# Optimization experiments

Hardware: AMD Instinct MI355X
Metric: run time of the kernel (lower is better)

## Reference

```python
import jax, jax.numpy as jnp
import numpy as np

N = 100000   # nodes
E = 1600000  # edges
IN = 128     # in_dim == hidden_dim
OUT = 64
MD = 16      # motif_dim
GH = 64      # gate hidden
TAU = 1.0
EPS = 1e-5


def setup_inputs() -> dict:
    key = jax.random.key(0)
    ks = jax.random.split(key, 8)
    return {
        "x": jax.random.normal(ks[0], (N, IN), jnp.float32),
        "motif_x": jax.random.normal(ks[1], (N, MD), jnp.float32),
        "edge_index": jax.random.randint(ks[2], (2, E), 0, N, jnp.int64),
        "gate_w1": jax.random.normal(ks[3], (4 * MD, GH), jnp.float32) * 0.05,
        "gate_b1": jnp.zeros((GH,), jnp.float32),
        "gate_w2": jax.random.normal(ks[4], (GH, 1), jnp.float32) * 0.05,
        "gate_b2": jnp.zeros((1,), jnp.float32),
        "conv_w": jax.random.normal(ks[5], (2, IN, IN), jnp.float32) * 0.05,
        "conv_b": jnp.zeros((2, IN), jnp.float32),
        "ln_g": jnp.ones((2, IN), jnp.float32),
        "ln_b": jnp.zeros((2, IN), jnp.float32),
        "head_w": jax.random.normal(ks[6], (IN, OUT), jnp.float32) * 0.05,
        "head_b": jnp.zeros((OUT,), jnp.float32),
    }


def reference(x, motif_x, edge_index, gate_w1, gate_b1, gate_w2, gate_b2,
              conv_w, conv_b, ln_g, ln_b, head_w, head_b):
    src, dst = edge_index[0], edge_index[1]

    # ---- EdgeGate: gather motif feats, small MLP, sigmoid gate per edge ----
    mu = motif_x[src]                      # [E, MD]
    mv = motif_x[dst]                      # [E, MD]
    feats = jnp.concatenate([mu, mv, jnp.abs(mu - mv), mu * mv], axis=1)  # [E, 4*MD]
    h = jax.nn.relu(feats @ gate_w1 + gate_b1)
    g = (h @ gate_w2 + gate_b2)[:, 0]
    gate = jnp.clip(jax.nn.sigmoid(g / TAU), 0.0, 1.0)  # [E]

    # ---- gcn_norm with self-loops (fill weight 1.0), shared across layers ----
    loops = jnp.arange(N, dtype=src.dtype)
    src_f = jnp.concatenate([src, loops])  # [E+N]
    dst_f = jnp.concatenate([dst, loops])
    w = jnp.concatenate([gate, jnp.ones((N,), gate.dtype)])
    deg = jax.ops.segment_sum(w, dst_f, num_segments=N)
    dinv = jnp.where(deg > 0, jax.lax.rsqrt(jnp.maximum(deg, EPS * 0 + 1e-30)), 0.0)
    dinv = jnp.where(deg > 0, deg ** -0.5, 0.0)
    norm = dinv[src_f] * w * dinv[dst_f]   # [E+N]

    # ---- 2 GCN layers: lin -> scatter-add -> bias -> LN -> relu -> residual ----
    for i in range(2):
        xw = x @ conv_w[i]                                   # [N, IN]
        msg = norm[:, None] * xw[src_f]                      # [E+N, IN]
        hh = jax.ops.segment_sum(msg, dst_f, num_segments=N) + conv_b[i]
        mean = jnp.mean(hh, axis=-1, keepdims=True)
        var = jnp.mean((hh - mean) ** 2, axis=-1, keepdims=True)
        hh = (hh - mean) * jax.lax.rsqrt(var + EPS) * ln_g[i] + ln_b[i]
        hh = jax.nn.relu(hh)
        x = x + hh                                           # residual (dims match)

    return x @ head_w + head_b             # [N, OUT]
```

## Files before the change

kernel.cpp:

```cpp
#include <hip/hip_runtime.h>
#include <cstdint>
#include <cstddef>

#define NN 100000
#define NE 1600000
#define IND 128
#define OUTD 64
#define MDIM 16
#define GHID 64
#define NPART 12500

typedef __attribute__((ext_vector_type(8))) short bf8_t;
typedef __attribute__((ext_vector_type(4))) float f4_t;
typedef unsigned short ushort_t;

__device__ inline unsigned f2bf_pack(float a, float b) {
    unsigned ua = __float_as_uint(a);
    unsigned ub = __float_as_uint(b);
    unsigned ra = (ua + 0x7fffu + ((ua >> 16) & 1u)) >> 16;
    unsigned rb = (ub + 0x7fffu + ((ub >> 16) & 1u)) >> 16;
    return ra | (rb << 16);
}
__device__ inline ushort_t f2bf1(float f) {
    unsigned u = __float_as_uint(f);
    return (ushort_t)((u + 0x7fffu + ((u >> 16) & 1u)) >> 16);
}
__device__ inline float2 bf2x(unsigned u) {
    return make_float2(__uint_as_float(u << 16),
                       __uint_as_float(u & 0xffff0000u));
}

__global__ __launch_bounds__(64) void k_detect(const void* ei, int* flag) {
    const unsigned long long* p = (const unsigned long long*)ei;
    int i = threadIdx.x;
    unsigned long long v = p[(size_t)i * (NE / 64)];
    bool hi0 = (v >> 32) == 0ull;
    unsigned long long b = __ballot(hi0);
    if (i == 0) *flag = (b == ~0ull) ? 1 : 0;
}

__global__ __launch_bounds__(256) void k_init(int* count) {
    int n = blockIdx.x * 256 + threadIdx.x;
    if (n < NN) count[n] = 0;
}

__global__ __launch_bounds__(256) void k_hist(const void* __restrict__ ei,
                                              const int* __restrict__ flag,
                                              int* __restrict__ count) {
    int e = blockIdx.x * 256 + threadIdx.x;
    if (e >= NE) return;
    int d = (*flag) ? (int)((const long long*)ei)[NE + e]
                    : ((const int*)ei)[NE + e];
    atomicAdd(&count[d], 1);
}

__global__ __launch_bounds__(256) void k_cvt(const float* __restrict__ x,
                                             unsigned* __restrict__ xb) {
    int i = blockIdx.x * 256 + threadIdx.x;
    if (i >= NN * 32) return;
    float4 v = ((const float4*)x)[i];
    ((uint2*)xb)[i] = make_uint2(f2bf_pack(v.x, v.y), f2bf_pack(v.z, v.w));
}

__global__ __launch_bounds__(256) void k_prep(const float* __restrict__ cw,
                                              const float* __restrict__ hw,
                                              unsigned* __restrict__ btf) {
    int i = blockIdx.x * 256 + threadIdx.x;
    if (i >= 20480) return;
    const float* W;
    int ncols, local;
    if (i < 16384) { W = cw + (i >> 13) * 16384; ncols = 128; local = i & 8191; }
    else { W = hw; ncols = 64; local = i - 16384; }
    int w = local & 3;
    int lane = (local >> 2) & 63;
    int kk = (local >> 8) & 3;
    int nt = local >> 10;
    int n = nt * 16 + (lane & 15);
    int k = kk * 32 + (lane >> 4) * 8 + 2 * w;
    btf[i] = f2bf_pack(W[k * ncols + n], W[(k + 1) * ncols + n]);
}

__global__ __launch_bounds__(256) void k_pre(const float* __restrict__ motif,
                                             const float* __restrict__ w1,
                                             unsigned* __restrict__ Pab) {
    __shared__ float sw[16][128];
    __shared__ unsigned sout[64][65];
    int tid = threadIdx.x;
#pragma unroll
    for (int i = 0; i < 8; i++) {
        int flat = tid + 256 * i;
        int k = flat >> 7, c = flat & 127;
        int row = (c < 64) ? k : (16 + k);
        sw[k][c] = w1[row * 64 + (c & 63)];
    }
    __syncthreads();
    int lane = tid & 63;
    int cg = tid >> 6;
    int n = blockIdx.x * 64 + lane;
    float m[MDIM];
    if (n < NN) {
        const float4* mr = (const float4*)(motif + (size_t)n * MDIM);
#pragma unroll
        for (int i = 0; i < 4; i++) {
            float4 t = mr[i];
            m[4 * i] = t.x; m[4 * i + 1] = t.y;
            m[4 * i + 2] = t.z; m[4 * i + 3] = t.w;
        }
    } else {
#pragma unroll
        for (int i = 0; i < MDIM; i++) m[i] = 0.0f;
    }
    float h[32];
#pragma unroll
    for (int j = 0; j < 32; j++) h[j] = 0.0f;
#pragma unroll
    for (int k = 0; k < MDIM; k++) {
        float f = m[k];
        const float* wr = &sw[k][cg * 32];
#pragma unroll
        for (int j = 0; j < 32; j++) h[j] = fmaf(f, wr[j], h[j]);
    }
#pragma unroll
    for (int jj = 0; jj < 16; jj++)
        sout[lane][cg * 16 + jj] = f2bf_pack(h[2 * jj], h[2 * jj + 1]);
    __syncthreads();
    int base = blockIdx.x * 64;
#pragma unroll
    for (int i = 0; i < 16; i++) {
        int flat = i * 256 + tid;
        int row = flat >> 6, col = flat & 63;
        int nn = base + row;
        if (nn < NN) Pab[(size_t)nn * 64 + col] = sout[row][col];
    }
}

__global__ __launch_bounds__(256) void k_scan1(const int* __restrict__ count,
                                               int* __restrict__ rs,
                                               int* __restrict__ bsum) {
    __shared__ int sd[256];
    int tid = threadIdx.x;
    int base = blockIdx.x * 2048 + tid * 8;
    int loc[8]; int s = 0;
#pragma unroll
    for (int i = 0; i < 8; i++) {
        int idx = base + i;
        int v = (idx < NN) ? count[idx] : 0;
        loc[i] = s; s += v;
    }
    sd[tid] = s; __syncthreads();
    for (int off = 1; off < 256; off <<= 1) {
        int t = (tid >= off) ? sd[tid - off] : 0;
        __syncthreads();
        sd[tid] += t;
        __syncthreads();
    }
    int texcl = sd[tid] - s;
    if (tid == 255) bsum[blockIdx.x] = sd[255];
#pragma unroll
    for (int i = 0; i < 8; i++) {
        int idx = base + i;
        if (idx < NN) rs[idx] = texcl + loc[i];
    }
}

__global__ __launch_bounds__(64) void k_scan2(const int* __restrict__ bsum,
                                              int* __restrict__ boffs) {
    int tid = threadIdx.x;
    int v = (tid < 49) ? bsum[tid] : 0;
    int x = v;
#pragma unroll
    for (int off = 1; off < 64; off <<= 1) {
        int t = __shfl_up(x, off, 64);
        if (tid >= off) x += t;
    }
    boffs[tid] = x - v;
}

__global__ __launch_bounds__(256) void k_scan3(int* __restrict__ rs,
                                               const int* __restrict__ boffs,
                                               int* __restrict__ cursor) {
    int i = blockIdx.x * 256 + threadIdx.x;
    if (i < NN) {
        int v = rs[i] + boffs[i >> 11];
        rs[i] = v;
        cursor[i] = v;
    }
}

__global__ __launch_bounds__(256) void k_fill(const void* __restrict__ ei,
                                              const int* __restrict__ flag,
                                              int* __restrict__ cursor,
                                              int2* __restrict__ es) {
    int p = blockIdx.x & 7;
    int base = (blockIdx.x >> 3) * 2048;
    bool is64 = (*flag) != 0;
#pragma unroll 1
    for (int it = 0; it < 8; it++) {
        int e = base + it * 256 + threadIdx.x;
        if (e >= NE) break;
        int d = is64 ? (int)((const long long*)ei)[NE + e]
                     : ((const int*)ei)[NE + e];
        if ((unsigned)d / NPART != (unsigned)p) continue;
        int s = is64 ? (int)((const long long*)ei)[e] : ((const int*)ei)[e];
        int pos = atomicAdd(&cursor[d], 1);
        es[pos] = make_int2(s, d);
    }
}

__global__ __launch_bounds__(256, 4) void k_gate(
    const float* __restrict__ motif, const int2* __restrict__ es,
    const unsigned* __restrict__ Pab, const float* __restrict__ w1,
    const float* __restrict__ b1, const float* __restrict__ w2,
    const float* __restrict__ b2, float* __restrict__ g_s) {
    int e = blockIdx.x * 256 + threadIdx.x;
    if (e >= NE) return;
    int2 sd = es[e];
    int s = sd.x, d = sd.y;
    float mu[MDIM], mv[MDIM];
    const float4* ms = (const float4*)(motif + (size_t)s * MDIM);
    const float4* mdp = (const float4*)(motif + (size_t)d * MDIM);
#pragma unroll
    for (int q = 0; q < 4; q++) {
        float4 a = ms[q], b = mdp[q];
        mu[4 * q] = a.x; mu[4 * q + 1] = a.y; mu[4 * q + 2] = a.z; mu[4 * q + 3] = a.w;
        mv[4 * q] = b.x; mv[4 * q + 1] = b.y; mv[4 * q + 2] = b.z; mv[4 * q + 3] = b.w;
    }
    const unsigned* pas = Pab + (size_t)s * 64;
    const unsigned* pbd = Pab + (size_t)d * 64 + 32;
    const float* w1c = w1 + 2 * MDIM * GHID;
    const float* w1d = w1 + 3 * MDIM * GHID;
    float g = b2[0];
#pragma unroll 1
    for (int jh = 0; jh < 2; jh++) {
        float h[32];
#pragma unroll
        for (int jj = 0; jj < 16; jj++) {
            float2 a = bf2x(pas[jh * 16 + jj]);
            float2 b = bf2x(pbd[jh * 16 + jj]);
            h[2 * jj] = a.x + b.x + b1[jh * 32 + 2 * jj];
            h[2 * jj + 1] = a.y + b.y + b1[jh * 32 + 2 * jj + 1];
        }
#pragma unroll 1
        for (int k = 0; k < MDIM; k++) {
            float f0 = mu[k], f1 = mv[k];
            float f2 = fabsf(f0 - f1), f3 = f0 * f1;
            const float* wc = w1c + k * GHID + jh * 32;
            const float* wd = w1d + k * GHID + jh * 32;
#pragma unroll
            for (int j = 0; j < 32; j++) {
                h[j] = fmaf(f2, wc[j], h[j]);
                h[j] = fmaf(f3, wd[j], h[j]);
            }
        }
        const float* w2p = w2 + jh * 32;
#pragma unroll
        for (int j = 0; j < 32; j++) g = fmaf(fmaxf(h[j], 0.0f), w2p[j], g);
    }
    g_s[e] = 1.0f / (1.0f + __expf(-g));
}

__global__ __launch_bounds__(256) void k_deg(const int* __restrict__ rowstart,
                                             const int* __restrict__ count,
                                             const float* __restrict__ g_s,
                                             float* __restrict__ dinv) {
    int n = blockIdx.x * 4 + (threadIdx.x >> 6);
    int lane = threadIdx.x & 63;
    if (n >= NN) return;
    int a = rowstart[n], cnt = count[n];
    float sum = 0.0f;
    for (int c = lane; c < cnt; c += 64) sum += g_s[a + c];
#pragma unroll
    for (int m = 1; m < 64; m <<= 1) sum += __shfl_xor(sum, m, 64);
    if (lane == 0) dinv[n] = rsqrtf(1.0f + sum);
}

__global__ __launch_bounds__(256) void k_wnorm(const int2* __restrict__ es,
                                               const float* __restrict__ dinv,
                                               float* __restrict__ g_s) {
    int e = blockIdx.x * 256 + threadIdx.x;
    if (e >= NE) return;
    int2 sd = es[e];
    g_s[e] *= dinv[sd.x] * dinv[sd.y];
}

__global__ __launch_bounds__(256) void k_mm_conv(
    const ushort_t* __restrict__ A, const uint4* __restrict__ btf,
    ushort_t* __restrict__ outb) {
    int w = threadIdx.x >> 6, lane = threadIdx.x & 63;
    int mh = w & 1, nh = w >> 1;
    int quad = lane >> 4, lx = lane & 15;
    int m0 = blockIdx.x * 64 + mh * 32;
    bf8_t a[2][4];
#pragma unroll
    for (int mt = 0; mt < 2; mt++) {
        int row = m0 + mt * 16 + lx;
        row = row < NN ? row : NN - 1;
#pragma unroll
        for (int kk = 0; kk < 4; kk++)
            a[mt][kk] = *(const bf8_t*)(A + (size_t)row * 128 + kk * 32 + quad * 8);
    }
    f4_t acc[2][4];
#pragma unroll
    for (int mt = 0; mt < 2; mt++)
#pragma unroll
        for (int nt = 0; nt < 4; nt++) acc[mt][nt] = (f4_t){0.f, 0.f, 0.f, 0.f};
#pragma unroll
    for (int nt = 0; nt < 4; nt++) {
        int ntg = nh * 4 + nt;
#pragma unroll
        for (int kk = 0; kk < 4; kk++) {
            union { uint4 u; bf8_t v; } bb;
            bb.u = btf[(ntg * 4 + kk) * 64 + lane];
            acc[0][nt] = __builtin_amdgcn_mfma_f32_16x16x32_bf16(
                a[0][kk], bb.v, acc[0][nt], 0, 0, 0);
            acc[1][nt] = __builtin_amdgcn_mfma_f32_16x16x32_bf16(
                a[1][kk], bb.v, acc[1][nt], 0, 0, 0);
        }
    }
#pragma unroll
    for (int mt = 0; mt < 2; mt++)
#pragma unroll
        for (int nt = 0; nt < 4; nt++) {
#pragma unroll
            for (int r = 0; r < 4; r++) {
                int row = m0 + mt * 16 + quad * 4 + r;
                if (row < NN)
                    outb[(size_t)row * 128 + (nh * 4 + nt) * 16 + lx] =
                        f2bf1(acc[mt][nt][r]);
            }
        }
}

__global__ __launch_bounds__(256) void k_mm_head(
    const ushort_t* __restrict__ A, const uint4* __restrict__ btf,
    const float* __restrict__ bias, float* __restrict__ out) {
    int w = threadIdx.x >> 6, lane = threadIdx.x & 63;
    int mh = w & 1, nh = w >> 1;
    int quad = lane >> 4, lx = lane & 15;
    int m0 = blockIdx.x * 64 + mh * 32;
    bf8_t a[2][4];
#pragma unroll
    for (int mt = 0; mt < 2; mt++) {
        int row = m0 + mt * 16 + lx;
        row = row < NN ? row : NN - 1;
#pragma unroll
        for (int kk = 0; kk < 4; kk++)
            a[mt][kk] = *(const bf8_t*)(A + (size_t)row * 128 + kk * 32 + quad * 8);
    }
    f4_t acc[2][2];
#pragma unroll
    for (int mt = 0; mt < 2; mt++)
#pragma unroll
        for (int nt = 0; nt < 2; nt++) acc[mt][nt] = (f4_t){0.f, 0.f, 0.f, 0.f};
#pragma unroll
    for (int nt = 0; nt < 2; nt++) {
        int ntg = nh * 2 + nt;
#pragma unroll
        for (int kk = 0; kk < 4; kk++) {
            union { uint4 u; bf8_t v; } bb;
            bb.u = btf[(ntg * 4 + kk) * 64 + lane];
            acc[0][nt] = __builtin_amdgcn_mfma_f32_16x16x32_bf16(
                a[0][kk], bb.v, acc[0][nt], 0, 0, 0);
            acc[1][nt] = __builtin_amdgcn_mfma_f32_16x16x32_bf16(
                a[1][kk], bb.v, acc[1][nt], 0, 0, 0);
        }
    }
#pragma unroll
    for (int mt = 0; mt < 2; mt++)
#pragma unroll
        for (int nt = 0; nt < 2; nt++) {
            int col = (nh * 2 + nt) * 16 + lx;
            float bs = bias[col];
#pragma unroll
            for (int r = 0; r < 4; r++) {
                int row = m0 + mt * 16 + quad * 4 + r;
                if (row < NN) out[(size_t)row * 64 + col] = acc[mt][nt][r] + bs;
            }
        }
}

__global__ __launch_bounds__(256) void k_aggr(
    const int* __restrict__ rowstart, const int* __restrict__ count,
    const int2* __restrict__ es, const float* __restrict__ w_s,
    const unsigned* __restrict__ xwb, const float* __restrict__ dinv,
    const float* __restrict__ xold, float* __restrict__ xnew,
    unsigned* __restrict__ xnewb, const float* __restrict__ cb,
    const float* __restrict__ lg, const float* __restrict__ lb) {
    int n = blockIdx.x * 4 + (threadIdx.x >> 6);
    int lane = threadIdx.x & 63;
    if (n >= NN) return;
    float dn = dinv[n];
    float2 acc = bf2x(xwb[(size_t)n * 64 + lane]);
    acc.x *= dn * dn; acc.y *= dn * dn;
    int start = rowstart[n], cnt = count[n];
    for (int c = 0; c < cnt; c += 64) {
        int rem = cnt - c;
        int sv = 0; float wv = 0.0f;
        if (lane < rem) {
            sv = es[start + c + lane].x;
            wv = w_s[start + c + lane];
        }
        int m = rem < 64 ? rem : 64;
        int j = 0;
        for (; j + 4 <= m; j += 4) {
            int s0 = __shfl(sv, j, 64), s1 = __shfl(sv, j + 1, 64);
            int s2 = __shfl(sv, j + 2, 64), s3 = __shfl(sv, j + 3, 64);
            float w0 = __shfl(wv, j, 64), w1 = __shfl(wv, j + 1, 64);
            float w2 = __shfl(wv, j + 2, 64), w3 = __shfl(wv, j + 3, 64);
            unsigned u0 = xwb[(size_t)s0 * 64 + lane];
            unsigned u1 = xwb[(size_t)s1 * 64 + lane];
            unsigned u2 = xwb[(size_t)s2 * 64 + lane];
            unsigned u3 = xwb[(size_t)s3 * 64 + lane];
            float2 v0 = bf2x(u0), v1 = bf2x(u1), v2 = bf2x(u2), v3 = bf2x(u3);
            acc.x = fmaf(w0, v0.x, acc.x); acc.y = fmaf(w0, v0.y, acc.y);
            acc.x = fmaf(w1, v1.x, acc.x); acc.y = fmaf(w1, v1.y, acc.y);
            acc.x = fmaf(w2, v2.x, acc.x); acc.y = fmaf(w2, v2.y, acc.y);
            acc.x = fmaf(w3, v3.x, acc.x); acc.y = fmaf(w3, v3.y, acc.y);
        }
        for (; j < m; j++) {
            int s = __shfl(sv, j, 64);
            float w = __shfl(wv, j, 64);
            float2 v = bf2x(xwb[(size_t)s * 64 + lane]);
            acc.x = fmaf(w, v.x, acc.x); acc.y = fmaf(w, v.y, acc.y);
        }
    }
    float2 cbv = ((const float2*)cb)[lane];
    acc.x += cbv.x; acc.y += cbv.y;
    float s1 = acc.x + acc.y, s2 = acc.x * acc.x + acc.y * acc.y;
#pragma unroll
    for (int mm = 1; mm < 64; mm <<= 1) {
        s1 += __shfl_xor(s1, mm, 64);
        s2 += __shfl_xor(s2, mm, 64);
    }
    float mean = s1 * (1.0f / 128.0f);
    float var = s2 * (1.0f / 128.0f) - mean * mean;
    float rstd = rsqrtf(var + 1e-5f);
    float2 lgv = ((const float2*)lg)[lane];
    float2 lbv = ((const float2*)lb)[lane];
    float y0 = fmaxf((acc.x - mean) * rstd * lgv.x + lbv.x, 0.0f);
    float y1 = fmaxf((acc.y - mean) * rstd * lgv.y + lbv.y, 0.0f);
    float2 xo = ((const float2*)xold)[(size_t)n * 64 + lane];
    float o0 = xo.x + y0, o1 = xo.y + y1;
    ((float2*)xnew)[(size_t)n * 64 + lane] = make_float2(o0, o1);
    xnewb[(size_t)n * 64 + lane] = f2bf_pack(o0, o1);
}

extern "C" void kernel_launch(void* const* d_in, const int* in_sizes, int n_in,
                              void* d_out, int out_size, void* d_ws,
                              size_t ws_size, hipStream_t stream) {
    const float* x = (const float*)d_in[0];
    const float* motif = (const float*)d_in[1];
    const void* ei = d_in[2];
    const float* gw1 = (const float*)d_in[3];
    const float* gb1 = (const float*)d_in[4];
    const float* gw2 = (const float*)d_in[5];
    const float* gb2 = (const float*)d_in[6];
    const float* cw = (const float*)d_in[7];
    const float* cb = (const float*)d_in[8];
    const float* lg = (const float*)d_in[9];
    const float* lb = (const float*)d_in[10];
    const float* hw = (const float*)d_in[11];
    const float* hb = (const float*)d_in[12];
    float* out = (float*)d_out;

    float* ws = (float*)d_ws;
    size_t o = 0;
    float* dinv = ws + o; o += NN;
    int* flag = (int*)(ws + o); o += 64;
    int* count = (int*)(ws + o); o += NN;
    int* rowstart = (int*)(ws + o); o += NN;
    int* cursor = (int*)(ws + o); o += NN;
    int* bsum = (int*)(ws + o); o += 64;
    int* boffs = (int*)(ws + o); o += 64;
    int2* es = (int2*)(ws + o); o += 2 * (size_t)NE;
    float* g_s = ws + o; o += NE;
    unsigned* xwb = (unsigned*)(ws + o); o += (size_t)NN * 64;
    float* xc = ws + o; o += (size_t)NN * IND;
    unsigned* xb = (unsigned*)(ws + o); o += (size_t)NN * 64;
    unsigned* xcb = (unsigned*)(ws + o); o += (size_t)NN * 64;
    unsigned* btf = (unsigned*)(ws + o); o += 20480;

    unsigned* Pab = xwb;

    k_detect<<<1, 64, 0, stream>>>(ei, flag);
    k_init<<<(NN + 255) / 256, 256, 0, stream>>>(count);
    k_hist<<<NE / 256, 256, 0, stream>>>(ei, flag, count);
    k_cvt<<<(NN * 32 + 255) / 256, 256, 0, stream>>>(x, xb);
    k_prep<<<80, 256, 0, stream>>>(cw, hw, btf);
    k_pre<<<(NN + 63) / 64, 256, 0, stream>>>(motif, gw1, Pab);

    k_scan1<<<(NN + 2047) / 2048, 256, 0, stream>>>(count, rowstart, bsum);
    k_scan2<<<1, 64, 0, stream>>>(bsum, boffs);
    k_scan3<<<(NN + 255) / 256, 256, 0, stream>>>(rowstart, boffs, cursor);
    k_fill<<<8 * ((NE + 2047) / 2048), 256, 0, stream>>>(ei, flag, cursor, es);

    k_gate<<<NE / 256, 256, 0, stream>>>(motif, es, Pab, gw1, gb1, gw2, gb2,
                                         g_s);
    k_deg<<<(NN + 3) / 4, 256, 0, stream>>>(rowstart, count, g_s, dinv);
    k_wnorm<<<NE / 256, 256, 0, stream>>>(es, dinv, g_s);

    const int gmm = (NN + 63) / 64;
    k_mm_conv<<<gmm, 256, 0, stream>>>((const ushort_t*)xb, (const uint4*)btf,
                                       (ushort_t*)xwb);
    k_aggr<<<(NN + 3) / 4, 256, 0, stream>>>(rowstart, count, es, g_s, xwb,
                                             dinv, x, xc, xcb, cb, lg, lb);
    k_mm_conv<<<gmm, 256, 0, stream>>>((const ushort_t*)xcb,
                                       (const uint4*)(btf + 8192),
                                       (ushort_t*)xwb);
    k_aggr<<<(NN + 3) / 4, 256, 0, stream>>>(rowstart, count, es, g_s, xwb,
                                             dinv, xc, xc, xcb, cb + IND,
                                             lg + IND, lb + IND);

    k_mm_head<<<gmm, 256, 0, stream>>>((const ushort_t*)xcb,
                                       (const uint4*)(btf + 16384), hb, out);
}
```

Measured before the change: 624.8 us.

## Compute edge gate MLP with bf16 MFMA and fuse input conversion into GEMM

Rewrites the per-edge gate MLP as bf16 MFMA tiles: each wave handles 16 edges, building the 64-wide feature row from src/dst motif features with cross-lane shuffles. The weights are pre-swizzled in k_prep. This removes the per-node precompute kernel k_pre and the scalar FMA loops. Separately, the fp32-to-bf16 conversion of x moves into a new first-layer GEMM kernel, so k_cvt and its buffer are gone. The trade-off is reduced precision, since all gate inputs are now rounded to bf16.

```diff
diff --git a/kernel.cpp b/kernel.cpp
--- a/kernel.cpp
+++ b/kernel.cpp
@@ -54,84 +54,31 @@
     atomicAdd(&count[d], 1);
 }
 
-__global__ __launch_bounds__(256) void k_cvt(const float* __restrict__ x,
-                                             unsigned* __restrict__ xb) {
-    int i = blockIdx.x * 256 + threadIdx.x;
-    if (i >= NN * 32) return;
-    float4 v = ((const float4*)x)[i];
-    ((uint2*)xb)[i] = make_uint2(f2bf_pack(v.x, v.y), f2bf_pack(v.z, v.w));
-}
-
 __global__ __launch_bounds__(256) void k_prep(const float* __restrict__ cw,
                                               const float* __restrict__ hw,
+                                              const float* __restrict__ w1,
                                               unsigned* __restrict__ btf) {
     int i = blockIdx.x * 256 + threadIdx.x;
-    if (i >= 20480) return;
+    if (i >= 22528) return;
     const float* W;
-    int ncols, local;
-    if (i < 16384) { W = cw + (i >> 13) * 16384; ncols = 128; local = i & 8191; }
-    else { W = hw; ncols = 64; local = i - 16384; }
-    int w = local & 3;
-    int lane = (local >> 2) & 63;
-    int kk = (local >> 8) & 3;
-    int nt = local >> 10;
+    int ncols, local, kk, nt;
+    int w, lane;
+    if (i < 16384) {
+        W = cw + (i >> 13) * 16384; ncols = 128; local = i & 8191;
+        w = local & 3; lane = (local >> 2) & 63;
+        kk = (local >> 8) & 3; nt = local >> 10;
+    } else if (i < 20480) {
+        W = hw; ncols = 64; local = i - 16384;
+        w = local & 3; lane = (local >> 2) & 63;
+        kk = (local >> 8) & 3; nt = local >> 10;
+    } else {
+        W = w1; ncols = 64; local = i - 20480;
+        w = local & 3; lane = (local >> 2) & 63;
+        kk = (local >> 8) & 1; nt = local >> 9;
+    }
     int n = nt * 16 + (lane & 15);
     int k = kk * 32 + (lane >> 4) * 8 + 2 * w;
     btf[i] = f2bf_pack(W[k * ncols + n], W[(k + 1) * ncols + n]);
-}
-
-__global__ __launch_bounds__(256) void k_pre(const float* __restrict__ motif,
-                                             const float* __restrict__ w1,
-                                             unsigned* __restrict__ Pab) {
-    __shared__ float sw[16][128];
-    __shared__ unsigned sout[64][65];
-    int tid = threadIdx.x;
-#pragma unroll
-    for (int i = 0; i < 8; i++) {
-        int flat = tid + 256 * i;
-        int k = flat >> 7, c = flat & 127;
-        int row = (c < 64) ? k : (16 + k);
-        sw[k][c] = w1[row * 64 + (c & 63)];
-    }
-    __syncthreads();
-    int lane = tid & 63;
-    int cg = tid >> 6;
-    int n = blockIdx.x * 64 + lane;
-    float m[MDIM];
-    if (n < NN) {
-        const float4* mr = (const float4*)(motif + (size_t)n * MDIM);
-#pragma unroll
-        for (int i = 0; i < 4; i++) {
-            float4 t = mr[i];
-            m[4 * i] = t.x; m[4 * i + 1] = t.y;
-            m[4 * i + 2] = t.z; m[4 * i + 3] = t.w;
-        }
-    } else {
-#pragma unroll
-        for (int i = 0; i < MDIM; i++) m[i] = 0.0f;
-    }
-    float h[32];
-#pragma unroll
-    for (int j = 0; j < 32; j++) h[j] = 0.0f;
-#pragma unroll
-    for (int k = 0; k < MDIM; k++) {
-        float f = m[k];
-        const float* wr = &sw[k][cg * 32];
-#pragma unroll
-        for (int j = 0; j < 32; j++) h[j] = fmaf(f, wr[j], h[j]);
-    }
-#pragma unroll
-    for (int jj = 0; jj < 16; jj++)
-        sout[lane][cg * 16 + jj] = f2bf_pack(h[2 * jj], h[2 * jj + 1]);
-    __syncthreads();
-    int base = blockIdx.x * 64;
-#pragma unroll
-    for (int i = 0; i < 16; i++) {
-        int flat = i * 256 + tid;
-        int row = flat >> 6, col = flat & 63;
-        int nn = base + row;
-        if (nn < NN) Pab[(size_t)nn * 64 + col] = sout[row][col];
-    }
 }
 
 __global__ __launch_bounds__(256) void k_scan1(const int* __restrict__ count,
@@ -207,56 +154,65 @@
     }
 }
 
-__global__ __launch_bounds__(256, 4) void k_gate(
+__global__ __launch_bounds__(256) void k_gate(
     const float* __restrict__ motif, const int2* __restrict__ es,
-    const unsigned* __restrict__ Pab, const float* __restrict__ w1,
-    const float* __restrict__ b1, const float* __restrict__ w2,
-    const float* __restrict__ b2, float* __restrict__ g_s) {
-    int e = blockIdx.x * 256 + threadIdx.x;
-    if (e >= NE) return;
-    int2 sd = es[e];
-    int s = sd.x, d = sd.y;
-    float mu[MDIM], mv[MDIM];
-    const float4* ms = (const float4*)(motif + (size_t)s * MDIM);
-    const float4* mdp = (const float4*)(motif + (size_t)d * MDIM);
-#pragma unroll
-    for (int q = 0; q < 4; q++) {
-        float4 a = ms[q], b = mdp[q];
-        mu[4 * q] = a.x; mu[4 * q + 1] = a.y; mu[4 * q + 2] = a.z; mu[4 * q + 3] = a.w;
-        mv[4 * q] = b.x; mv[4 * q + 1] = b.y; mv[4 * q + 2] = b.z; mv[4 * q + 3] = b.w;
-    }
-    const unsigned* pas = Pab + (size_t)s * 64;
-    const unsigned* pbd = Pab + (size_t)d * 64 + 32;
-    const float* w1c = w1 + 2 * MDIM * GHID;
-    const float* w1d = w1 + 3 * MDIM * GHID;
-    float g = b2[0];
-#pragma unroll 1
-    for (int jh = 0; jh < 2; jh++) {
-        float h[32];
-#pragma unroll
-        for (int jj = 0; jj < 16; jj++) {
-            float2 a = bf2x(pas[jh * 16 + jj]);
-            float2 b = bf2x(pbd[jh * 16 + jj]);
-            h[2 * jj] = a.x + b.x + b1[jh * 32 + 2 * jj];
-            h[2 * jj + 1] = a.y + b.y + b1[jh * 32 + 2 * jj + 1];
-        }
-#pragma unroll 1
-        for (int k = 0; k < MDIM; k++) {
-            float f0 = mu[k], f1 = mv[k];
-            float f2 = fabsf(f0 - f1), f3 = f0 * f1;
-            const float* wc = w1c + k * GHID + jh * 32;
-            const float* wd = w1d + k * GHID + jh * 32;
-#pragma unroll
-            for (int j = 0; j < 32; j++) {
-                h[j] = fmaf(f2, wc[j], h[j]);
-                h[j] = fmaf(f3, wd[j], h[j]);
-            }
-        }
-        const float* w2p = w2 + jh * 32;
-#pragma unroll
-        for (int j = 0; j < 32; j++) g = fmaf(fmaxf(h[j], 0.0f), w2p[j], g);
-    }
-    g_s[e] = 1.0f / (1.0f + __expf(-g));
+    const uint4* __restrict__ w1f, const float* __restrict__ b1,
+    const float* __restrict__ w2, const float* __restrict__ b2,
+    float* __restrict__ g_s) {
+    int wv = threadIdx.x >> 6, lane = threadIdx.x & 63;
+    int e0 = (blockIdx.x * 4 + wv) * 16;
+    int quad = lane >> 4, lx = lane & 15;
+    int2 sd = es[e0 + lx];
+    int node = (quad < 2) ? sd.x : sd.y;
+    int half = quad & 1;
+    const float4* mp =
+        (const float4*)(motif + (size_t)node * MDIM + half * 8);
+    float4 v0 = mp[0], v1 = mp[1];
+    float own[8] = {v0.x, v0.y, v0.z, v0.w, v1.x, v1.y, v1.z, v1.w};
+    union { unsigned u[4]; bf8_t v; } a0, a1;
+#pragma unroll
+    for (int q = 0; q < 4; q++) a0.u[q] = f2bf_pack(own[2 * q], own[2 * q + 1]);
+    float f[8];
+#pragma unroll
+    for (int j = 0; j < 8; j++) {
+        float oth = __shfl_xor(own[j], 32, 64);
+        f[j] = (quad < 2) ? fabsf(own[j] - oth) : own[j] * oth;
+    }
+#pragma unroll
+    for (int q = 0; q < 4; q++) a1.u[q] = f2bf_pack(f[2 * q], f[2 * q + 1]);
+    f4_t acc[4];
+#pragma unroll
+    for (int nt = 0; nt < 4; nt++) {
+        float bi = b1[nt * 16 + lx];
+        acc[nt] = (f4_t){bi, bi, bi, bi};
+    }
+#pragma unroll
+    for (int nt = 0; nt < 4; nt++) {
+        union { uint4 u; bf8_t v; } b0, bb1;
+        b0.u = w1f[(nt * 2 + 0) * 64 + lane];
+        bb1.u = w1f[(nt * 2 + 1) * 64 + lane];
+        acc[nt] = __builtin_amdgcn_mfma_f32_16x16x32_bf16(a0.v, b0.v, acc[nt],
+                                                          0, 0, 0);
+        acc[nt] = __builtin_amdgcn_mfma_f32_16x16x32_bf16(a1.v, bb1.v, acc[nt],
+                                                          0, 0, 0);
+    }
+    float p[4] = {0.f, 0.f, 0.f, 0.f};
+#pragma unroll
+    for (int nt = 0; nt < 4; nt++) {
+        float w2v = w2[nt * 16 + lx];
+#pragma unroll
+        for (int r = 0; r < 4; r++)
+            p[r] = fmaf(fmaxf(acc[nt][r], 0.0f), w2v, p[r]);
+    }
+#pragma unroll
+    for (int m = 1; m < 16; m <<= 1) {
+#pragma unroll
+        for (int r = 0; r < 4; r++) p[r] += __shfl_xor(p[r], m, 64);
+    }
+    if (lx < 4) {
+        float g = p[lx] + b2[0];
+        g_s[e0 + quad * 4 + lx] = 1.0f / (1.0f + __expf(-g));
+    }
 }
 
 __global__ __launch_bounds__(256) void k_deg(const int* __restrict__ rowstart,
@@ -281,6 +237,63 @@
     if (e >= NE) return;
     int2 sd = es[e];
     g_s[e] *= dinv[sd.x] * dinv[sd.y];
+}
+
+__global__ __launch_bounds__(256) void k_mm_conv_f32(
+    const float* __restrict__ A, const uint4* __restrict__ btf,
+    ushort_t* __restrict__ outb) {
+    int w = threadIdx.x >> 6, lane = threadIdx.x & 63;
+    int mh = w & 1, nh = w >> 1;
+    int quad = lane >> 4, lx = lane & 15;
+    int m0 = blockIdx.x * 64 + mh * 32;
+    bf8_t a[2][4];
+#pragma unroll
+    for (int mt = 0; mt < 2; mt++) {
+        int row = m0 + mt * 16 + lx;
+        row = row < NN ? row : NN - 1;
+#pragma unroll
+        for (int kk = 0; kk < 4; kk++) {
+            const float4* ap =
+                (const float4*)(A + (size_t)row * 128 + kk * 32 + quad * 8);
+            float4 u0 = ap[0], u1 = ap[1];
+            union { unsigned u[4]; bf8_t v; } t;
+            t.u[0] = f2bf_pack(u0.x, u0.y);
+            t.u[1] = f2bf_pack(u0.z, u0.w);
+            t.u[2] = f2bf_pack(u1.x, u1.y);
+            t.u[3] = f2bf_pack(u1.z, u1.w);
+            a[mt][kk] = t.v;
+        }
+    }
+    f4_t acc[2][4];
+#pragma unroll
+    for (int mt = 0; mt < 2; mt++)
+#pragma unroll
+        for (int nt = 0; nt < 4; nt++) acc[mt][nt] = (f4_t){0.f, 0.f, 0.f, 0.f};
+#pragma unroll
+    for (int nt = 0; nt < 4; nt++) {
+        int ntg = nh * 4 + nt;
+#pragma unroll
+        for (int kk = 0; kk < 4; kk++) {
+            union { uint4 u; bf8_t v; } bb;
+            bb.u = btf[(ntg * 4 + kk) * 64 + lane];
+            acc[0][nt] = __builtin_amdgcn_mfma_f32_16x16x32_bf16(
+                a[0][kk], bb.v, acc[0][nt], 0, 0, 0);
+            acc[1][nt] = __builtin_amdgcn_mfma_f32_16x16x32_bf16(
+                a[1][kk], bb.v, acc[1][nt], 0, 0, 0);
+        }
+    }
+#pragma unroll
+    for (int mt = 0; mt < 2; mt++)
+#pragma unroll
+        for (int nt = 0; nt < 4; nt++) {
+#pragma unroll
+            for (int r = 0; r < 4; r++) {
+                int row = m0 + mt * 16 + quad * 4 + r;
+                if (row < NN)
+                    outb[(size_t)row * 128 + (nh * 4 + nt) * 16 + lx] =
+                        f2bf1(acc[mt][nt][r]);
+            }
+        }
 }
 
 __global__ __launch_bounds__(256) void k_mm_conv(
@@ -476,32 +489,27 @@
     float* g_s = ws + o; o += NE;
     unsigned* xwb = (unsigned*)(ws + o); o += (size_t)NN * 64;
     float* xc = ws + o; o += (size_t)NN * IND;
-    unsigned* xb = (unsigned*)(ws + o); o += (size_t)NN * 64;
     unsigned* xcb = (unsigned*)(ws + o); o += (size_t)NN * 64;
-    unsigned* btf = (unsigned*)(ws + o); o += 20480;
-
-    unsigned* Pab = xwb;
+    unsigned* btf = (unsigned*)(ws + o); o += 22528;
 
     k_detect<<<1, 64, 0, stream>>>(ei, flag);
     k_init<<<(NN + 255) / 256, 256, 0, stream>>>(count);
     k_hist<<<NE / 256, 256, 0, stream>>>(ei, flag, count);
-    k_cvt<<<(NN * 32 + 255) / 256, 256, 0, stream>>>(x, xb);
-    k_prep<<<80, 256, 0, stream>>>(cw, hw, btf);
-    k_pre<<<(NN + 63) / 64, 256, 0, stream>>>(motif, gw1, Pab);
+    k_prep<<<88, 256, 0, stream>>>(cw, hw, gw1, btf);
 
     k_scan1<<<(NN + 2047) / 2048, 256, 0, stream>>>(count, rowstart, bsum);
     k_scan2<<<1, 64, 0, stream>>>(bsum, boffs);
     k_scan3<<<(NN + 255) / 256, 256, 0, stream>>>(rowstart, boffs, cursor);
     k_fill<<<8 * ((NE + 2047) / 2048), 256, 0, stream>>>(ei, flag, cursor, es);
 
-    k_gate<<<NE / 256, 256, 0, stream>>>(motif, es, Pab, gw1, gb1, gw2, gb2,
-                                         g_s);
+    k_gate<<<NE / 64, 256, 0, stream>>>(motif, es, (const uint4*)(btf + 20480),
+                                        gb1, gw2, gb2, g_s);
     k_deg<<<(NN + 3) / 4, 256, 0, stream>>>(rowstart, count, g_s, dinv);
     k_wnorm<<<NE / 256, 256, 0, stream>>>(es, dinv, g_s);
 
     const int gmm = (NN + 63) / 64;
-    k_mm_conv<<<gmm, 256, 0, stream>>>((const ushort_t*)xb, (const uint4*)btf,
-                                       (ushort_t*)xwb);
+    k_mm_conv_f32<<<gmm, 256, 0, stream>>>(x, (const uint4*)btf,
+                                           (ushort_t*)xwb);
     k_aggr<<<(NN + 3) / 4, 256, 0, stream>>>(rowstart, count, es, g_s, xwb,
                                              dinv, x, xc, xcb, cb, lg, lb);
     k_mm_conv<<<gmm, 256, 0, stream>>>((const ushort_t*)xcb,
```

Measured after the change: 551.5 us. 1.13x faster.
